# Kernel optimization log

Hardware: AMD Instinct MI355X
Metric: run time of the kernel (lower is better)

## Reference

```python
import jax, jax.numpy as jnp
import numpy as np

N = 100000   # nodes
E = 640000   # edges
G = 256      # graphs in batch
L = 3        # mpnn layers
D_IN = 64    # in_node_channels
E_IN = 16    # in_edge_channels
H = 128      # hidden width (uniform)


def setup_inputs() -> dict:
    key = jax.random.key(0)
    ks = jax.random.split(key, 20)
    s = 0.05
    inp = {
        "x": jax.random.normal(ks[0], (N, D_IN), dtype=jnp.float32),
        "edge_index": jax.random.randint(ks[1], (2, E), 0, N, dtype=jnp.int64),
        "edge_attr": jax.random.normal(ks[2], (E, E_IN), dtype=jnp.float32),
        "batch_vec": jnp.sort(jax.random.randint(ks[3], (N,), 0, G, dtype=jnp.int64)),
        # input encoders
        "Wn0": jax.random.normal(ks[4], (D_IN, H), dtype=jnp.float32) * s,
        "bn0": jnp.zeros((H,), jnp.float32),
        "We0": jax.random.normal(ks[5], (E_IN, H), dtype=jnp.float32) * s,
        "be0": jnp.zeros((H,), jnp.float32),
        # per-layer MPNN params (stacked over L)
        "WM": jax.random.normal(ks[6], (L, 3 * H, H), dtype=jnp.float32) * s,
        "bM": jnp.zeros((L, H), jnp.float32),
        "WU": jax.random.normal(ks[7], (L, 2 * H, H), dtype=jnp.float32) * s,
        "bU": jnp.zeros((L, H), jnp.float32),
        # per-layer node/edge linear layers
        "Wn": jax.random.normal(ks[8], (L, H, H), dtype=jnp.float32) * s,
        "bn": jnp.zeros((L, H), jnp.float32),
        "We": jax.random.normal(ks[9], (L, H, H), dtype=jnp.float32) * s,
        "be": jnp.zeros((L, H), jnp.float32),
        "Wh": jax.random.normal(ks[10], (H, 1), dtype=jnp.float32) * s,
        "bh": jnp.zeros((1,), jnp.float32),
    }
    return inp


def _mpnn_layer(x, edge_attr, src, dst, WM, bM, WU, bU):
    # message: relu(Linear([x_i, x_j, e]))  (x_i = target, x_j = source)
    xi = x[dst]                                   # [E, H]
    xj = x[src]                                   # [E, H]
    m = jax.nn.relu(jnp.concatenate([xi, xj, edge_attr], axis=-1) @ WM + bM)
    # mean aggregation at target nodes
    agg = jax.ops.segment_sum(m, dst, num_segments=N)        # [N, H]
    cnt = jax.ops.segment_sum(jnp.ones((m.shape[0], 1), x.dtype), dst,
                              num_segments=N)
    agg = agg / jnp.maximum(cnt, 1.0)
    # update: relu(Linear([x, aggr_out]))
    return jax.nn.relu(jnp.concatenate([x, agg], axis=-1) @ WU + bU)


def reference(x, edge_index, edge_attr, batch_vec,
              Wn0, bn0, We0, be0, WM, bM, WU, bU, Wn, bn, We, be, Wh, bh):
    src, dst = edge_index[0], edge_index[1]       # PyG source_to_target flow
    h = jax.nn.relu(x @ Wn0 + bn0)                # NodeFeatureLinear
    e = jax.nn.relu(edge_attr @ We0 + be0)        # EdgeFeatureLinear
    for i in range(L):
        h = _mpnn_layer(h, e, src, dst, WM[i], bM[i], WU[i], bU[i])
        h = jax.nn.relu(h @ Wn[i] + bn[i])
        e = jax.nn.relu(e @ We[i] + be[i])
    # global mean pool over graphs
    sums = jax.ops.segment_sum(h, batch_vec, num_segments=G)  # [G, H]
    cnts = jax.ops.segment_sum(jnp.ones((N, 1), h.dtype), batch_vec,
                               num_segments=G)
    pooled = sums / jnp.maximum(cnts, 1.0)
    return pooled @ Wh + bh                       # [G, 1]
```

## Files before the change

### kernel.cpp

```cpp
#include <hip/hip_runtime.h>

#define NN 100000
#define EE 640000
#define GG 256
#define LL 3
#define HH 128

constexpr int BM = 64;
constexpr int BK = 16;

typedef _Float16 f16;
typedef f16 f16x8 __attribute__((ext_vector_type(8)));
typedef f16 f16x4 __attribute__((ext_vector_type(4)));
typedef f16 f16x2 __attribute__((ext_vector_type(2)));
typedef float f32x4 __attribute__((ext_vector_type(4)));

#define TSTR 136

__device__ __forceinline__ void gload_lds16(const void* g, void* l) {
  __builtin_amdgcn_global_load_lds(
      (const __attribute__((address_space(1))) void*)g,
      (__attribute__((address_space(3))) void*)l, 16, 0, 0);
}

template <int MODE>
__global__ __launch_bounds__(256) void gemm_k(
    const float* __restrict__ X, const float* __restrict__ W,
    const float* __restrict__ bias, float* __restrict__ out, int M, int K,
    const float* __restrict__ X2, const float* __restrict__ inv) {
  __shared__ __align__(16) float Xs[BK][BM];
  __shared__ __align__(16) float Ws[BK][HH];

  const int tid = threadIdx.x;
  const int m0 = blockIdx.x * BM;
  const int tm = (tid >> 4) << 2;
  const int tn = (tid & 15) << 3;
  const int xr = tid >> 2;
  const int xc = (tid & 3) << 2;

  float acc[4][8];
#pragma unroll
  for (int i = 0; i < 4; ++i)
#pragma unroll
    for (int j = 0; j < 8; ++j) acc[i][j] = 0.f;

  for (int k0 = 0; k0 < K; k0 += BK) {
    float4 xv = make_float4(0.f, 0.f, 0.f, 0.f);
    if (m0 + xr < M) {
      if (MODE == 3) {
        if (k0 < HH) {
          xv = *(const float4*)(X + (size_t)(m0 + xr) * HH + k0 + xc);
        } else {
          xv = *(const float4*)(X2 + (size_t)(m0 + xr) * HH + (k0 - HH) + xc);
          const float s = inv[m0 + xr];
          xv.x *= s; xv.y *= s; xv.z *= s; xv.w *= s;
        }
      } else {
        xv = *(const float4*)(X + (size_t)(m0 + xr) * K + k0 + xc);
      }
    }
    Xs[xc + 0][xr] = xv.x;
    Xs[xc + 1][xr] = xv.y;
    Xs[xc + 2][xr] = xv.z;
    Xs[xc + 3][xr] = xv.w;
#pragma unroll
    for (int i = 0; i < 2; ++i) {
      const int q = tid + i * 256;
      const int row = q >> 5;
      const int c4 = (q & 31) << 2;
      *(float4*)&Ws[row][c4] =
          *(const float4*)(W + (size_t)(k0 + row) * HH + c4);
    }
    __syncthreads();
#pragma unroll
    for (int k = 0; k < BK; ++k) {
      const float4 x4 = *(const float4*)&Xs[k][tm];
      const float4 w0 = *(const float4*)&Ws[k][tn];
      const float4 w1 = *(const float4*)&Ws[k][tn + 4];
      const float xr_[4] = {x4.x, x4.y, x4.z, x4.w};
      const float wr_[8] = {w0.x, w0.y, w0.z, w0.w, w1.x, w1.y, w1.z, w1.w};
#pragma unroll
      for (int i = 0; i < 4; ++i)
#pragma unroll
        for (int j = 0; j < 8; ++j)
          acc[i][j] = fmaf(xr_[i], wr_[j], acc[i][j]);
    }
    __syncthreads();
  }

#pragma unroll
  for (int i = 0; i < 4; ++i) {
    const int r = m0 + tm + i;
    if (r >= M) continue;
    float o[8];
#pragma unroll
    for (int j = 0; j < 8; ++j) {
      float v = acc[i][j];
      if (MODE == 1 || MODE == 3) {
        v += bias[tn + j];
        v = v > 0.f ? v : 0.f;
      }
      o[j] = v;
    }
    float4* d4 = (float4*)(out + (size_t)r * HH + tn);
    d4[0] = make_float4(o[0], o[1], o[2], o[3]);
    d4[1] = make_float4(o[4], o[5], o[6], o[7]);
  }
}

__global__ void prep_w(const float* __restrict__ We0,
                       const float* __restrict__ We,
                       const float* __restrict__ WM,
                       const float* __restrict__ Wn0,
                       const float* __restrict__ Wn,
                       const float* __restrict__ WU, f16* __restrict__ out) {
  const int buf = blockIdx.x >> 3;
  const int rowg = blockIdx.x & 7;
  const float* src;
  int K;
  if (buf == 0) {
    src = We0; K = 16;
  } else if (buf <= 2) {
    src = We + (size_t)(buf - 1) * HH * HH; K = HH;
  } else if (buf <= 5) {
    src = WM + (size_t)(buf - 3) * 3 * HH * HH + 2 * HH * HH; K = HH;
  } else if (buf == 6) {
    src = Wn0; K = 64;
  } else if (buf <= 9) {
    src = WM + (size_t)(buf - 7) * 3 * HH * HH; K = HH;
  } else if (buf <= 12) {
    src = WM + (size_t)(buf - 10) * 3 * HH * HH + HH * HH; K = HH;
  } else if (buf <= 15) {
    src = Wn + (size_t)(buf - 13) * HH * HH; K = HH;
  } else {
    const int t = buf - 16;
    src = WU + (size_t)(t >> 1) * 2 * HH * HH + (size_t)(t & 1) * HH * HH;
    K = HH;
  }
  f16* dst = out + (size_t)buf * HH * TSTR;
  for (int idx = threadIdx.x; idx < 16 * TSTR; idx += 256) {
    const int n = rowg * 16 + idx / TSTR;
    const int k = idx % TSTR;
    const float v = (k < K) ? src[(size_t)k * HH + n] : 0.f;
    dst[(size_t)n * TSTR + k] = (f16)v;
  }
}

template <int MODE>
__global__ __launch_bounds__(256) void gemm_mfma(
    const float* __restrict__ X, const f16* __restrict__ WT,
    const float* __restrict__ bias, float* __restrict__ out, int M,
    const float* __restrict__ X2, const float* __restrict__ inv,
    const f16* __restrict__ WT2, float* __restrict__ out2) {
  __shared__ __align__(16) char smem[17408 + 34816];
  f16* Xs = (f16*)smem;
  f16* Wt = (f16*)(smem + 17408);
  float* V = (float*)(smem + 17408);

  const int tid = threadIdx.x;
  const int lane = tid & 63;
  const int wv = tid >> 6;
  const int l15 = lane & 15;
  const int q = lane >> 4;
  const int m0 = blockIdx.x * 64;

  f32x4 acc[4][2];
#pragma unroll
  for (int mi = 0; mi < 4; ++mi)
#pragma unroll
    for (int ni = 0; ni < 2; ++ni) {
      f32x4 z = {};
      acc[mi][ni] = z;
    }

  auto stageX = [&](const float* Xp, int stride, int KC, bool scale) {
    const int npr = KC >> 2;
    for (int i = tid; i < 64 * npr; i += 256) {
      const int row = i / npr;
      const int c4 = (i - row * npr) << 2;
      float4 v = make_float4(0.f, 0.f, 0.f, 0.f);
      if (m0 + row < M) {
        v = *(const float4*)(Xp + (size_t)(m0 + row) * stride + c4);
        if (scale) {
          const float s = inv[m0 + row];
          v.x *= s; v.y *= s; v.z *= s; v.w *= s;
        }
      }
      f16x4 hv;
      hv[0] = (f16)v.x; hv[1] = (f16)v.y; hv[2] = (f16)v.z; hv[3] = (f16)v.w;
      *(f16x4*)&Xs[(size_t)row * TSTR + c4] = hv;
    }
  };

  auto stageX16 = [&](const f16* Xp) {
    for (int i = tid; i < 1024; i += 256) {
      const int row = i >> 4;
      const int c8 = (i & 15) << 3;
      f16x8 v = {};
      if (m0 + row < M) v = *(const f16x8*)(Xp + (size_t)(m0 + row) * HH + c8);
      *(f16x8*)&Xs[(size_t)row * TSTR + c8] = v;
    }
  };

  auto stageW = [&](const f16* Wg) {
    const char* g = (const char*)Wg;
    char* l = (char*)Wt;
#pragma unroll
    for (int i = 0; i < 8; ++i)
      gload_lds16(g + tid * 16 + i * 4096, l + tid * 16 + i * 4096);
    if (tid < 128) gload_lds16(g + tid * 16 + 32768, l + tid * 16 + 32768);
  };

  auto mfmaN = [&](f32x4 (&ac)[4][2], int nk) {
    for (int kk = 0; kk < nk; ++kk) {
      f16x8 a[4], b[2];
#pragma unroll
      for (int mi = 0; mi < 4; ++mi)
        a[mi] = *(const f16x8*)&Xs[(size_t)(mi * 16 + l15) * TSTR + kk * 32 +
                                   q * 8];
#pragma unroll
      for (int ni = 0; ni < 2; ++ni)
        b[ni] = *(const f16x8*)&Wt[(size_t)((wv * 2 + ni) * 16 + l15) * TSTR +
                                   kk * 32 + q * 8];
#pragma unroll
      for (int mi = 0; mi < 4; ++mi)
#pragma unroll
        for (int ni = 0; ni < 2; ++ni)
          ac[mi][ni] = __builtin_amdgcn_mfma_f32_16x16x32_f16(
              a[mi], b[ni], ac[mi][ni], 0, 0, 0);
    }
  };

  auto dumpV = [&](f32x4 (&ac)[4][2], const float* bp) {
    float bv0 = 0.f, bv1 = 0.f;
    if (bp) { bv0 = bp[wv * 32 + l15]; bv1 = bp[wv * 32 + 16 + l15]; }
#pragma unroll
    for (int mi = 0; mi < 4; ++mi)
#pragma unroll
      for (int ni = 0; ni < 2; ++ni)
#pragma unroll
        for (int rr = 0; rr < 4; ++rr) {
          float v = ac[mi][ni][rr];
          if (bp) {
            v += ni ? bv1 : bv0;
            v = v > 0.f ? v : 0.f;
          }
          V[(size_t)(mi * 16 + q * 4 + rr) * 132 + wv * 32 + ni * 16 + l15] =
              v;
        }
  };

  auto storeV16 = [&](f16* op) {
    const int tm = (tid >> 4) << 2;
    const int tn = (tid & 15) << 3;
#pragma unroll
    for (int i = 0; i < 4; ++i) {
      const int r = m0 + tm + i;
      if (r >= M) continue;
      const float* vp = &V[(size_t)(tm + i) * 132 + tn];
      f16x8 hv;
#pragma unroll
      for (int j = 0; j < 8; ++j) hv[j] = (f16)vp[j];
      *(f16x8*)(op + (size_t)r * HH + tn) = hv;
    }
  };

  if constexpr (MODE == 2) {
    stageW(WT);
    stageX(X, 64, 64, false);
    __syncthreads();
    mfmaN(acc, 2);
    __syncthreads();
    dumpV(acc, bias);
    __syncthreads();
    storeV16((f16*)out);
  } else if constexpr (MODE == 1) {
    stageW(WT);
    stageX16((const f16*)X);
    __syncthreads();
    mfmaN(acc, 4);
    __syncthreads();
    dumpV(acc, bias);
    __syncthreads();
    storeV16((f16*)out);
  } else if constexpr (MODE == 3) {
    stageW(WT);
    stageX16((const f16*)X);
    __syncthreads();
    mfmaN(acc, 4);
    __syncthreads();
    stageW(WT + (size_t)HH * TSTR);
    stageX(X2, HH, 128, true);
    __syncthreads();
    mfmaN(acc, 4);
    __syncthreads();
    dumpV(acc, bias);
    __syncthreads();
    storeV16((f16*)out);
  } else {
    f32x4 acc2[4][2];
#pragma unroll
    for (int mi = 0; mi < 4; ++mi)
#pragma unroll
      for (int ni = 0; ni < 2; ++ni) {
        f32x4 z = {};
        acc2[mi][ni] = z;
      }
    stageW(WT);
    stageX16((const f16*)X);
    __syncthreads();
    mfmaN(acc, 4);
    __syncthreads();
    stageW(WT2);
    __syncthreads();
    mfmaN(acc2, 4);
    __syncthreads();
    dumpV(acc, nullptr);
    __syncthreads();
    storeV16((f16*)out);
    __syncthreads();
    dumpV(acc2, nullptr);
    __syncthreads();
    storeV16((f16*)out2);
  }
}

template <int CHAIN>
__global__ __launch_bounds__(512) void msg_k(
    const float* __restrict__ ea, const f16* __restrict__ W0T,
    const float* __restrict__ be0, const f16* __restrict__ WeT,
    const float* __restrict__ beL, const f16* __restrict__ WMeT,
    const float* __restrict__ bMl, const f16* __restrict__ A,
    const f16* __restrict__ B, const int* __restrict__ sIdx,
    const int* __restrict__ sSrc, const int* __restrict__ sDst,
    float* __restrict__ agg) {
  __shared__ __align__(16) char smem[34816 + 34816 + 512];
  f16* Tc = (f16*)smem;
  f16* Wc = (f16*)(smem + 34816);
  float* V = (float*)smem;
  int* dstS = (int*)(smem + 69632);

  const int tid = threadIdx.x;
  const int lane = tid & 63;
  const int wv = tid >> 6;
  const int ew = (wv >> 2) * 64;
  const int wn = wv & 3;
  const int l15 = lane & 15;
  const int q = lane >> 4;
  const int r0 = blockIdx.x * 128;

  auto wptr = [&](int p) -> const f16* {
    if (p == 0) return W0T;
    if (p <= CHAIN) return WeT + (size_t)(p - 1) * HH * TSTR;
    return WMeT;
  };

  auto stage_w = [&](const f16* Wg) {
    const char* g = (const char*)Wg;
    char* l = (char*)Wc;
#pragma unroll
    for (int i = 0; i < 4; ++i)
      gload_lds16(g + tid * 16 + i * 8192, l + tid * 16 + i * 8192);
    if (tid < 128) gload_lds16(g + tid * 16 + 32768, l + tid * 16 + 32768);
  };

  stage_w(wptr(0));
  {
    const int xr = tid >> 2;
    const int xc = (tid & 3) << 2;
    const int e = sIdx[r0 + xr];
    const float4 v = *(const float4*)(ea + (size_t)e * 16 + xc);
    f16x4 hv;
    hv[0] = (f16)v.x; hv[1] = (f16)v.y; hv[2] = (f16)v.z; hv[3] = (f16)v.w;
    *(f16x4*)&Tc[(size_t)xr * TSTR + xc] = hv;
    f16x4 z = {};
    *(f16x4*)&Tc[(size_t)xr * TSTR + 16 + xc] = z;
    if (tid < 128) dstS[tid] = sDst[r0 + tid];
  }

  f32x4 acc[4][2];

  auto zero_acc = [&]() {
#pragma unroll
    for (int mi = 0; mi < 4; ++mi)
#pragma unroll
      for (int ni = 0; ni < 2; ++ni) {
        f32x4 z = {};
        acc[mi][ni] = z;
      }
  };

  auto mfma_steps = [&](int nk) {
    for (int kk = 0; kk < nk; ++kk) {
      f16x8 a[4], b[2];
#pragma unroll
      for (int mi = 0; mi < 4; ++mi)
        a[mi] = *(const f16x8*)&Tc[(size_t)(ew + mi * 16 + l15) * TSTR +
                                   kk * 32 + q * 8];
#pragma unroll
      for (int ni = 0; ni < 2; ++ni)
        b[ni] = *(const f16x8*)&Wc[(size_t)((wn * 2 + ni) * 16 + l15) * TSTR +
                                   kk * 32 + q * 8];
#pragma unroll
      for (int mi = 0; mi < 4; ++mi)
#pragma unroll
        for (int ni = 0; ni < 2; ++ni)
          acc[mi][ni] = __builtin_amdgcn_mfma_f32_16x16x32_f16(
              a[mi], b[ni], acc[mi][ni], 0, 0, 0);
    }
  };

  auto relu_body = [&](const float* bias) {
    float bv0 = bias[wn * 32 + l15];
    float bv1 = bias[wn * 32 + 16 + l15];
#pragma unroll
    for (int mi = 0; mi < 4; ++mi)
#pragma unroll
      for (int ni = 0; ni < 2; ++ni) {
        const float bb = ni ? bv1 : bv0;
#pragma unroll
        for (int rr = 0; rr < 4; ++rr) {
          float v = acc[mi][ni][rr] + bb;
          v = v > 0.f ? v : 0.f;
          Tc[(size_t)(ew + mi * 16 + q * 4 + rr) * TSTR + wn * 32 + ni * 16 +
             l15] = (f16)v;
        }
      }
  };

  zero_acc();
  __syncthreads();
  mfma_steps(1);
  __syncthreads();
  stage_w(wptr(1));
  relu_body(be0);
  __syncthreads();

#pragma unroll
  for (int s = 0; s < CHAIN; ++s) {
    zero_acc();
    mfma_steps(4);
    __syncthreads();
    stage_w(wptr(s + 2));
    relu_body(beL + (size_t)s * HH);
    __syncthreads();
  }

  zero_acc();
  mfma_steps(4);
  __syncthreads();

#pragma unroll
  for (int mi = 0; mi < 4; ++mi)
#pragma unroll
    for (int ni = 0; ni < 2; ++ni)
#pragma unroll
      for (int rr = 0; rr < 4; ++rr)
        V[(size_t)(ew + mi * 16 + q * 4 + rr) * 129 + wn * 32 + ni * 16 +
          l15] = acc[mi][ni][rr];
  __syncthreads();

  const int tm = (tid >> 4) << 2;
  const int tn = (tid & 15) << 3;
  const float4 m0v = *(const float4*)(bMl + tn);
  const float4 m1v = *(const float4*)(bMl + tn + 4);
  const float mv[8] = {m0v.x, m0v.y, m0v.z, m0v.w,
                       m1v.x, m1v.y, m1v.z, m1v.w};
#pragma unroll
  for (int i = 0; i < 4; ++i) {
    const int rr = r0 + tm + i;
    const int d = dstS[tm + i];
    const int s = sSrc[rr];
    const f16x8 a8 = *(const f16x8*)(A + (size_t)d * HH + tn);
    const f16x8 b8 = *(const f16x8*)(B + (size_t)s * HH + tn);
    float* vp = &V[(size_t)(tm + i) * 129 + tn];
#pragma unroll
    for (int j = 0; j < 8; ++j)
      vp[j] = fmaxf(vp[j] + (float)a8[j] + (float)b8[j] + mv[j], 0.f);
  }
  __syncthreads();

  const int c = tid & 127;
  const int h = tid >> 7;
  float racc = 0.f;
  int cur = dstS[h * 32];
  bool first = true;
  for (int e2 = h * 32; e2 < h * 32 + 32; ++e2) {
    const int d = dstS[e2];
    if (d != cur) {
      if (first) {
        atomicAdd(&agg[(size_t)cur * HH + c], racc);
        first = false;
      } else {
        agg[(size_t)cur * HH + c] = racc;
      }
      racc = 0.f;
      cur = d;
    }
    racc += V[(size_t)e2 * 129 + c];
  }
  atomicAdd(&agg[(size_t)cur * HH + c], racc);
}

__global__ void count_kernel(const int* __restrict__ dst, int* cnt, int E) {
  const int i = blockIdx.x * 256 + threadIdx.x;
  if (i < E) atomicAdd(&cnt[dst[i]], 1);
}

__global__ void invcnt_kernel(const int* __restrict__ cnt, float* inv, int n) {
  const int i = blockIdx.x * 256 + threadIdx.x;
  if (i < n) inv[i] = 1.0f / (float)max(cnt[i], 1);
}

__global__ void scan_block(const int* __restrict__ cnt, int* excl, int* bsum,
                           int n) {
  __shared__ int s[256];
  const int tx = threadIdx.x;
  const int i = blockIdx.x * 256 + tx;
  const int v = (i < n) ? cnt[i] : 0;
  s[tx] = v;
  __syncthreads();
  for (int off = 1; off < 256; off <<= 1) {
    int tv = (tx >= off) ? s[tx - off] : 0;
    __syncthreads();
    s[tx] += tv;
    __syncthreads();
  }
  if (i < n) excl[i] = s[tx] - v;
  if (tx == 255) bsum[blockIdx.x] = s[255];
}

__global__ __launch_bounds__(512) void scan_bsum(int* bsum, int nb) {
  __shared__ int s[512];
  const int t = threadIdx.x;
  const int v0 = (t < nb) ? bsum[t] : 0;
  s[t] = v0;
  __syncthreads();
  for (int off = 1; off < 512; off <<= 1) {
    const int tv = (t >= off) ? s[t - off] : 0;
    __syncthreads();
    s[t] += tv;
    __syncthreads();
  }
  if (t < nb) bsum[t] = s[t] - v0;
}

__global__ void scan_add(int* excl, const int* __restrict__ bsum, int n) {
  const int i = blockIdx.x * 256 + threadIdx.x;
  if (i < n) excl[i] += bsum[blockIdx.x];
}

__global__ void scatter_edges(const int* __restrict__ dst,
                              const int* __restrict__ src,
                              const int* __restrict__ off, int* ctr, int* sIdx,
                              int* sSrc, int* sDst, int E) {
  const int e = blockIdx.x * 256 + threadIdx.x;
  if (e >= E) return;
  const int d = dst[e];
  const int p = off[d] + atomicAdd(&ctr[d], 1);
  sIdx[p] = e;
  sSrc[p] = src[e];
  sDst[p] = d;
}

__global__ void pool_accum(const f16* __restrict__ h,
                           const int* __restrict__ batch,
                           float* __restrict__ gsum, int M) {
  const int col = threadIdx.x;
  const int r0 = blockIdx.x * 64;
  const int rend = min(r0 + 64, M);
  if (r0 >= M) return;
  float acc = 0.f;
  int cur = batch[r0];
  for (int r = r0; r < rend; ++r) {
    const int b = batch[r];
    if (b != cur) {
      atomicAdd(&gsum[(size_t)cur * HH + col], acc);
      acc = 0.f;
      cur = b;
    }
    acc += (float)h[(size_t)r * HH + col];
  }
  atomicAdd(&gsum[(size_t)cur * HH + col], acc);
}

__global__ void gcnt_kernel(const int* __restrict__ batch, int* gcnt, int n) {
  const int i = blockIdx.x * 256 + threadIdx.x;
  if (i < n) atomicAdd(&gcnt[batch[i]], 1);
}

__global__ void head_kernel(const float* __restrict__ gsum,
                            const int* __restrict__ gcnt,
                            const float* __restrict__ Wh,
                            const float* __restrict__ bh,
                            float* __restrict__ out) {
  const int g = blockIdx.x;
  const int t = threadIdx.x;
  float v = gsum[(size_t)g * HH + t] * Wh[t];
#pragma unroll
  for (int o = 32; o > 0; o >>= 1) v += __shfl_down(v, o, 64);
  __shared__ float red[2];
  if ((t & 63) == 0) red[t >> 6] = v;
  __syncthreads();
  if (t == 0) {
    const float s = red[0] + red[1];
    const float c = (float)max(gcnt[g], 1);
    out[g] = s / c + bh[0];
  }
}

extern "C" void kernel_launch(void* const* d_in, const int* in_sizes, int n_in,
                              void* d_out, int out_size, void* d_ws,
                              size_t ws_size, hipStream_t stream) {
  (void)in_sizes; (void)n_in; (void)out_size;
  const float* x = (const float*)d_in[0];
  const int* ei = (const int*)d_in[1];
  const float* ea = (const float*)d_in[2];
  const int* batch = (const int*)d_in[3];
  const float* Wn0 = (const float*)d_in[4];
  const float* bn0 = (const float*)d_in[5];
  const float* We0 = (const float*)d_in[6];
  const float* be0 = (const float*)d_in[7];
  const float* WM = (const float*)d_in[8];
  const float* bM = (const float*)d_in[9];
  const float* WU = (const float*)d_in[10];
  const float* bU = (const float*)d_in[11];
  const float* Wn = (const float*)d_in[12];
  const float* bn = (const float*)d_in[13];
  const float* We = (const float*)d_in[14];
  const float* be = (const float*)d_in[15];
  const float* Wh = (const float*)d_in[16];
  const float* bh = (const float*)d_in[17];

  const int* srcI = ei;
  const int* dstI = ei + EE;

  float* w = (float*)d_ws;
  size_t o = 0;
  f16* h16 = (f16*)(w + o);  o += (size_t)NN * HH / 2;
  float* agg = w + o;  o += (size_t)NN * HH;
  f16* A16 = (f16*)(w + o); o += (size_t)NN * HH / 2;
  f16* B16 = (f16*)(w + o); o += (size_t)NN * HH / 2;
  float* gsum = w + o; o += (size_t)GG * HH;
  float* invc = w + o; o += (size_t)NN;
  int* cnt = (int*)(w + o);  o += (size_t)NN;
  int* gcnt = (int*)(w + o); o += (size_t)GG;
  int* off = (int*)(w + o);  o += (size_t)NN;
  int* ctr = (int*)(w + o);  o += (size_t)NN;
  int* bsum = (int*)(w + o); o += 512;
  int* sIdx = (int*)(w + o); o += (size_t)EE;
  int* sSrc = (int*)(w + o); o += (size_t)EE;
  int* sDst = (int*)(w + o); o += (size_t)EE;
  f16* Wp = (f16*)(w + o);   o += (size_t)22 * HH * TSTR / 2;
  if (o * sizeof(float) > ws_size) return;

  auto WB = [&](int i) { return Wp + (size_t)i * HH * TSTR; };

  const dim3 blk(256);
  const int gridN = (NN + BM - 1) / BM;
  const int gridE = EE / 128;
  const int NBLK = (NN + 255) / 256;

  hipMemsetAsync(cnt, 0, (size_t)NN * sizeof(int), stream);
  hipMemsetAsync(ctr, 0, (size_t)NN * sizeof(int), stream);
  hipMemsetAsync(gsum, 0, (size_t)GG * HH * sizeof(float), stream);
  hipMemsetAsync(gcnt, 0, (size_t)GG * sizeof(int), stream);

  count_kernel<<<(EE + 255) / 256, blk, 0, stream>>>(dstI, cnt, EE);
  scan_block<<<NBLK, blk, 0, stream>>>(cnt, off, bsum, NN);
  scan_bsum<<<1, dim3(512), 0, stream>>>(bsum, NBLK);
  scan_add<<<NBLK, blk, 0, stream>>>(off, bsum, NN);
  scatter_edges<<<(EE + 255) / 256, blk, 0, stream>>>(dstI, srcI, off, ctr,
                                                      sIdx, sSrc, sDst, EE);
  invcnt_kernel<<<(NN + 255) / 256, blk, 0, stream>>>(cnt, invc, NN);
  prep_w<<<22 * 8, blk, 0, stream>>>(We0, We, WM, Wn0, Wn, WU, Wp);

  gemm_mfma<2><<<gridN, blk, 0, stream>>>(x, WB(6), bn0, (float*)h16, NN,
                                          nullptr, nullptr, nullptr, nullptr);

  for (int l = 0; l < LL; ++l) {
    gemm_mfma<4><<<gridN, blk, 0, stream>>>((const float*)h16, WB(7 + l),
                                            nullptr, (float*)A16, NN, nullptr,
                                            nullptr, WB(10 + l), (float*)B16);
    hipMemsetAsync(agg, 0, (size_t)NN * HH * sizeof(float), stream);
    switch (l) {
      case 0:
        msg_k<0><<<gridE, dim3(512), 0, stream>>>(
            ea, WB(0), be0, WB(1), be, WB(3), bM + 0 * HH, A16, B16, sIdx,
            sSrc, sDst, agg);
        break;
      case 1:
        msg_k<1><<<gridE, dim3(512), 0, stream>>>(
            ea, WB(0), be0, WB(1), be, WB(4), bM + 1 * HH, A16, B16, sIdx,
            sSrc, sDst, agg);
        break;
      default:
        msg_k<2><<<gridE, dim3(512), 0, stream>>>(
            ea, WB(0), be0, WB(1), be, WB(5), bM + 2 * HH, A16, B16, sIdx,
            sSrc, sDst, agg);
        break;
    }
    gemm_mfma<3><<<gridN, blk, 0, stream>>>((const float*)h16,
                                            WB(16 + 2 * l), bU + l * HH,
                                            (float*)h16, NN, agg, invc,
                                            nullptr, nullptr);
    gemm_mfma<1><<<gridN, blk, 0, stream>>>((const float*)h16, WB(13 + l),
                                            bn + l * HH, (float*)h16, NN,
                                            nullptr, nullptr, nullptr,
                                            nullptr);
  }

  pool_accum<<<gridN, dim3(128), 0, stream>>>(h16, batch, gsum, NN);
  gcnt_kernel<<<(NN + 255) / 256, blk, 0, stream>>>(batch, gcnt, NN);
  head_kernel<<<GG, dim3(128), 0, stream>>>(gsum, gcnt, Wh, bh, (float*)d_out);
}
```

Baseline: 1.035 ms.

## Fuse node GEMM chain (update, node linear, next-layer projections) into one kernel

Replaces the separate per-layer node GEMM launches (update, node linear, next layer's A/B projections) with one fused kernel per layer, plus a fused encoder+projection kernel. Intermediate h stays in LDS as fp16 between GEMMs instead of round-tripping through global memory, and kernel launches drop. Each block now runs more sequential GEMM stages with extra barriers, and the in-place h16 write-back relies on row-local dependence only.

```diff
diff --git a/kernel.cpp b/kernel.cpp
--- a/kernel.cpp
+++ b/kernel.cpp
@@ -21,91 +21,6 @@
   __builtin_amdgcn_global_load_lds(
       (const __attribute__((address_space(1))) void*)g,
       (__attribute__((address_space(3))) void*)l, 16, 0, 0);
-}
-
-template <int MODE>
-__global__ __launch_bounds__(256) void gemm_k(
-    const float* __restrict__ X, const float* __restrict__ W,
-    const float* __restrict__ bias, float* __restrict__ out, int M, int K,
-    const float* __restrict__ X2, const float* __restrict__ inv) {
-  __shared__ __align__(16) float Xs[BK][BM];
-  __shared__ __align__(16) float Ws[BK][HH];
-
-  const int tid = threadIdx.x;
-  const int m0 = blockIdx.x * BM;
-  const int tm = (tid >> 4) << 2;
-  const int tn = (tid & 15) << 3;
-  const int xr = tid >> 2;
-  const int xc = (tid & 3) << 2;
-
-  float acc[4][8];
-#pragma unroll
-  for (int i = 0; i < 4; ++i)
-#pragma unroll
-    for (int j = 0; j < 8; ++j) acc[i][j] = 0.f;
-
-  for (int k0 = 0; k0 < K; k0 += BK) {
-    float4 xv = make_float4(0.f, 0.f, 0.f, 0.f);
-    if (m0 + xr < M) {
-      if (MODE == 3) {
-        if (k0 < HH) {
-          xv = *(const float4*)(X + (size_t)(m0 + xr) * HH + k0 + xc);
-        } else {
-          xv = *(const float4*)(X2 + (size_t)(m0 + xr) * HH + (k0 - HH) + xc);
-          const float s = inv[m0 + xr];
-          xv.x *= s; xv.y *= s; xv.z *= s; xv.w *= s;
-        }
-      } else {
-        xv = *(const float4*)(X + (size_t)(m0 + xr) * K + k0 + xc);
-      }
-    }
-    Xs[xc + 0][xr] = xv.x;
-    Xs[xc + 1][xr] = xv.y;
-    Xs[xc + 2][xr] = xv.z;
-    Xs[xc + 3][xr] = xv.w;
-#pragma unroll
-    for (int i = 0; i < 2; ++i) {
-      const int q = tid + i * 256;
-      const int row = q >> 5;
-      const int c4 = (q & 31) << 2;
-      *(float4*)&Ws[row][c4] =
-          *(const float4*)(W + (size_t)(k0 + row) * HH + c4);
-    }
-    __syncthreads();
-#pragma unroll
-    for (int k = 0; k < BK; ++k) {
-      const float4 x4 = *(const float4*)&Xs[k][tm];
-      const float4 w0 = *(const float4*)&Ws[k][tn];
-      const float4 w1 = *(const float4*)&Ws[k][tn + 4];
-      const float xr_[4] = {x4.x, x4.y, x4.z, x4.w};
-      const float wr_[8] = {w0.x, w0.y, w0.z, w0.w, w1.x, w1.y, w1.z, w1.w};
-#pragma unroll
-      for (int i = 0; i < 4; ++i)
-#pragma unroll
-        for (int j = 0; j < 8; ++j)
-          acc[i][j] = fmaf(xr_[i], wr_[j], acc[i][j]);
-    }
-    __syncthreads();
-  }
-
-#pragma unroll
-  for (int i = 0; i < 4; ++i) {
-    const int r = m0 + tm + i;
-    if (r >= M) continue;
-    float o[8];
-#pragma unroll
-    for (int j = 0; j < 8; ++j) {
-      float v = acc[i][j];
-      if (MODE == 1 || MODE == 3) {
-        v += bias[tn + j];
-        v = v > 0.f ? v : 0.f;
-      }
-      o[j] = v;
-    }
-    float4* d4 = (float4*)(out + (size_t)r * HH + tn);
-    d4[0] = make_float4(o[0], o[1], o[2], o[3]);
-    d4[1] = make_float4(o[4], o[5], o[6], o[7]);
-  }
 }
 
 __global__ void prep_w(const float* __restrict__ We0,
@@ -146,183 +61,227 @@
   }
 }
 
-template <int MODE>
-__global__ __launch_bounds__(256) void gemm_mfma(
-    const float* __restrict__ X, const f16* __restrict__ WT,
-    const float* __restrict__ bias, float* __restrict__ out, int M,
-    const float* __restrict__ X2, const float* __restrict__ inv,
-    const f16* __restrict__ WT2, float* __restrict__ out2) {
-  __shared__ __align__(16) char smem[17408 + 34816];
-  f16* Xs = (f16*)smem;
-  f16* Wt = (f16*)(smem + 17408);
-  float* V = (float*)(smem + 17408);
-
-  const int tid = threadIdx.x;
-  const int lane = tid & 63;
-  const int wv = tid >> 6;
-  const int l15 = lane & 15;
-  const int q = lane >> 4;
-  const int m0 = blockIdx.x * 64;
-
-  f32x4 acc[4][2];
+struct GemmCtx {
+  f16* Xs; f16* Wt; float* V;
+  int tid, lane, wv, l15, q, m0;
+};
+
+__device__ __forceinline__ void ctx_init(GemmCtx& c, char* smem) {
+  c.Xs = (f16*)smem;
+  c.Wt = (f16*)(smem + 17408);
+  c.V = (float*)(smem + 17408);
+  c.tid = threadIdx.x;
+  c.lane = c.tid & 63;
+  c.wv = c.tid >> 6;
+  c.l15 = c.lane & 15;
+  c.q = c.lane >> 4;
+  c.m0 = blockIdx.x * 64;
+}
+
+__device__ __forceinline__ void c_stageW(GemmCtx& c, const f16* Wg) {
+  const char* g = (const char*)Wg;
+  char* l = (char*)c.Wt;
+#pragma unroll
+  for (int i = 0; i < 8; ++i)
+    gload_lds16(g + c.tid * 16 + i * 4096, l + c.tid * 16 + i * 4096);
+  if (c.tid < 128) gload_lds16(g + c.tid * 16 + 32768, l + c.tid * 16 + 32768);
+}
+
+__device__ __forceinline__ void c_stageXf32(GemmCtx& c, const float* Xp,
+                                            int stride, int KC, bool scale,
+                                            const float* inv, int M) {
+  const int npr = KC >> 2;
+  for (int i = c.tid; i < 64 * npr; i += 256) {
+    const int row = i / npr;
+    const int c4 = (i - row * npr) << 2;
+    float4 v = make_float4(0.f, 0.f, 0.f, 0.f);
+    if (c.m0 + row < M) {
+      v = *(const float4*)(Xp + (size_t)(c.m0 + row) * stride + c4);
+      if (scale) {
+        const float s = inv[c.m0 + row];
+        v.x *= s; v.y *= s; v.z *= s; v.w *= s;
+      }
+    }
+    f16x4 hv;
+    hv[0] = (f16)v.x; hv[1] = (f16)v.y; hv[2] = (f16)v.z; hv[3] = (f16)v.w;
+    *(f16x4*)&c.Xs[(size_t)row * TSTR + c4] = hv;
+  }
+}
+
+__device__ __forceinline__ void c_stageX16(GemmCtx& c, const f16* Xp, int M) {
+  for (int i = c.tid; i < 1024; i += 256) {
+    const int row = i >> 4;
+    const int c8 = (i & 15) << 3;
+    f16x8 v = {};
+    if (c.m0 + row < M) v = *(const f16x8*)(Xp + (size_t)(c.m0 + row) * HH + c8);
+    *(f16x8*)&c.Xs[(size_t)row * TSTR + c8] = v;
+  }
+}
+
+__device__ __forceinline__ void c_mfmaN(GemmCtx& c, f32x4 (&ac)[4][2],
+                                        int nk) {
+  for (int kk = 0; kk < nk; ++kk) {
+    f16x8 a[4], b[2];
+#pragma unroll
+    for (int mi = 0; mi < 4; ++mi)
+      a[mi] = *(const f16x8*)&c.Xs[(size_t)(mi * 16 + c.l15) * TSTR + kk * 32 +
+                                   c.q * 8];
+#pragma unroll
+    for (int ni = 0; ni < 2; ++ni)
+      b[ni] = *(const f16x8*)&c.Wt[(size_t)((c.wv * 2 + ni) * 16 + c.l15) *
+                                       TSTR +
+                                   kk * 32 + c.q * 8];
+#pragma unroll
+    for (int mi = 0; mi < 4; ++mi)
+#pragma unroll
+      for (int ni = 0; ni < 2; ++ni)
+        ac[mi][ni] = __builtin_amdgcn_mfma_f32_16x16x32_f16(a[mi], b[ni],
+                                                            ac[mi][ni], 0, 0,
+                                                            0);
+  }
+}
+
+__device__ __forceinline__ void c_zero(f32x4 (&ac)[4][2]) {
 #pragma unroll
   for (int mi = 0; mi < 4; ++mi)
 #pragma unroll
     for (int ni = 0; ni < 2; ++ni) {
       f32x4 z = {};
-      acc[mi][ni] = z;
-    }
-
-  auto stageX = [&](const float* Xp, int stride, int KC, bool scale) {
-    const int npr = KC >> 2;
-    for (int i = tid; i < 64 * npr; i += 256) {
-      const int row = i / npr;
-      const int c4 = (i - row * npr) << 2;
-      float4 v = make_float4(0.f, 0.f, 0.f, 0.f);
-      if (m0 + row < M) {
-        v = *(const float4*)(Xp + (size_t)(m0 + row) * stride + c4);
-        if (scale) {
-          const float s = inv[m0 + row];
-          v.x *= s; v.y *= s; v.z *= s; v.w *= s;
-        }
+      ac[mi][ni] = z;
+    }
+}
+
+__device__ __forceinline__ void c_reluXs(GemmCtx& c, f32x4 (&ac)[4][2],
+                                         const float* bias) {
+  const float bv0 = bias[c.wv * 32 + c.l15];
+  const float bv1 = bias[c.wv * 32 + 16 + c.l15];
+#pragma unroll
+  for (int mi = 0; mi < 4; ++mi)
+#pragma unroll
+    for (int ni = 0; ni < 2; ++ni) {
+      const float bb = ni ? bv1 : bv0;
+#pragma unroll
+      for (int rr = 0; rr < 4; ++rr) {
+        float v = ac[mi][ni][rr] + bb;
+        v = v > 0.f ? v : 0.f;
+        c.Xs[(size_t)(mi * 16 + c.q * 4 + rr) * TSTR + c.wv * 32 + ni * 16 +
+             c.l15] = (f16)v;
       }
-      f16x4 hv;
-      hv[0] = (f16)v.x; hv[1] = (f16)v.y; hv[2] = (f16)v.z; hv[3] = (f16)v.w;
-      *(f16x4*)&Xs[(size_t)row * TSTR + c4] = hv;
-    }
-  };
-
-  auto stageX16 = [&](const f16* Xp) {
-    for (int i = tid; i < 1024; i += 256) {
-      const int row = i >> 4;
-      const int c8 = (i & 15) << 3;
-      f16x8 v = {};
-      if (m0 + row < M) v = *(const f16x8*)(Xp + (size_t)(m0 + row) * HH + c8);
-      *(f16x8*)&Xs[(size_t)row * TSTR + c8] = v;
-    }
-  };
-
-  auto stageW = [&](const f16* Wg) {
-    const char* g = (const char*)Wg;
-    char* l = (char*)Wt;
-#pragma unroll
-    for (int i = 0; i < 8; ++i)
-      gload_lds16(g + tid * 16 + i * 4096, l + tid * 16 + i * 4096);
-    if (tid < 128) gload_lds16(g + tid * 16 + 32768, l + tid * 16 + 32768);
-  };
-
-  auto mfmaN = [&](f32x4 (&ac)[4][2], int nk) {
-    for (int kk = 0; kk < nk; ++kk) {
-      f16x8 a[4], b[2];
-#pragma unroll
-      for (int mi = 0; mi < 4; ++mi)
-        a[mi] = *(const f16x8*)&Xs[(size_t)(mi * 16 + l15) * TSTR + kk * 32 +
-                                   q * 8];
-#pragma unroll
-      for (int ni = 0; ni < 2; ++ni)
-        b[ni] = *(const f16x8*)&Wt[(size_t)((wv * 2 + ni) * 16 + l15) * TSTR +
-                                   kk * 32 + q * 8];
-#pragma unroll
-      for (int mi = 0; mi < 4; ++mi)
-#pragma unroll
-        for (int ni = 0; ni < 2; ++ni)
-          ac[mi][ni] = __builtin_amdgcn_mfma_f32_16x16x32_f16(
-              a[mi], b[ni], ac[mi][ni], 0, 0, 0);
-    }
-  };
-
-  auto dumpV = [&](f32x4 (&ac)[4][2], const float* bp) {
-    float bv0 = 0.f, bv1 = 0.f;
-    if (bp) { bv0 = bp[wv * 32 + l15]; bv1 = bp[wv * 32 + 16 + l15]; }
-#pragma unroll
-    for (int mi = 0; mi < 4; ++mi)
-#pragma unroll
-      for (int ni = 0; ni < 2; ++ni)
-#pragma unroll
-        for (int rr = 0; rr < 4; ++rr) {
-          float v = ac[mi][ni][rr];
-          if (bp) {
-            v += ni ? bv1 : bv0;
-            v = v > 0.f ? v : 0.f;
-          }
-          V[(size_t)(mi * 16 + q * 4 + rr) * 132 + wv * 32 + ni * 16 + l15] =
-              v;
-        }
-  };
-
-  auto storeV16 = [&](f16* op) {
-    const int tm = (tid >> 4) << 2;
-    const int tn = (tid & 15) << 3;
-#pragma unroll
-    for (int i = 0; i < 4; ++i) {
-      const int r = m0 + tm + i;
-      if (r >= M) continue;
-      const float* vp = &V[(size_t)(tm + i) * 132 + tn];
-      f16x8 hv;
-#pragma unroll
-      for (int j = 0; j < 8; ++j) hv[j] = (f16)vp[j];
-      *(f16x8*)(op + (size_t)r * HH + tn) = hv;
-    }
-  };
-
-  if constexpr (MODE == 2) {
-    stageW(WT);
-    stageX(X, 64, 64, false);
-    __syncthreads();
-    mfmaN(acc, 2);
-    __syncthreads();
-    dumpV(acc, bias);
-    __syncthreads();
-    storeV16((f16*)out);
-  } else if constexpr (MODE == 1) {
-    stageW(WT);
-    stageX16((const f16*)X);
-    __syncthreads();
-    mfmaN(acc, 4);
-    __syncthreads();
-    dumpV(acc, bias);
-    __syncthreads();
-    storeV16((f16*)out);
-  } else if constexpr (MODE == 3) {
-    stageW(WT);
-    stageX16((const f16*)X);
-    __syncthreads();
-    mfmaN(acc, 4);
-    __syncthreads();
-    stageW(WT + (size_t)HH * TSTR);
-    stageX(X2, HH, 128, true);
-    __syncthreads();
-    mfmaN(acc, 4);
-    __syncthreads();
-    dumpV(acc, bias);
-    __syncthreads();
-    storeV16((f16*)out);
-  } else {
-    f32x4 acc2[4][2];
-#pragma unroll
-    for (int mi = 0; mi < 4; ++mi)
-#pragma unroll
-      for (int ni = 0; ni < 2; ++ni) {
-        f32x4 z = {};
-        acc2[mi][ni] = z;
-      }
-    stageW(WT);
-    stageX16((const f16*)X);
-    __syncthreads();
-    mfmaN(acc, 4);
-    __syncthreads();
-    stageW(WT2);
-    __syncthreads();
-    mfmaN(acc2, 4);
-    __syncthreads();
-    dumpV(acc, nullptr);
-    __syncthreads();
-    storeV16((f16*)out);
-    __syncthreads();
-    dumpV(acc2, nullptr);
-    __syncthreads();
-    storeV16((f16*)out2);
-  }
+    }
+}
+
+__device__ __forceinline__ void c_dumpV(GemmCtx& c, f32x4 (&ac)[4][2]) {
+#pragma unroll
+  for (int mi = 0; mi < 4; ++mi)
+#pragma unroll
+    for (int ni = 0; ni < 2; ++ni)
+#pragma unroll
+      for (int rr = 0; rr < 4; ++rr)
+        c.V[(size_t)(mi * 16 + c.q * 4 + rr) * 132 + c.wv * 32 + ni * 16 +
+            c.l15] = ac[mi][ni][rr];
+}
+
+__device__ __forceinline__ void c_storeV16(GemmCtx& c, f16* op, int M) {
+  const int tm = (c.tid >> 4) << 2;
+  const int tn = (c.tid & 15) << 3;
+#pragma unroll
+  for (int i = 0; i < 4; ++i) {
+    const int r = c.m0 + tm + i;
+    if (r >= M) continue;
+    const float* vp = &c.V[(size_t)(tm + i) * 132 + tn];
+    f16x8 hv;
+#pragma unroll
+    for (int j = 0; j < 8; ++j) hv[j] = (f16)vp[j];
+    *(f16x8*)(op + (size_t)r * HH + tn) = hv;
+  }
+}
+
+__device__ __forceinline__ void c_storeXs16(GemmCtx& c, f16* op, int M) {
+  const int tm = (c.tid >> 4) << 2;
+  const int tn = (c.tid & 15) << 3;
+#pragma unroll
+  for (int i = 0; i < 4; ++i) {
+    const int r = c.m0 + tm + i;
+    if (r >= M) continue;
+    *(f16x8*)(op + (size_t)r * HH + tn) =
+        *(const f16x8*)&c.Xs[(size_t)(tm + i) * TSTR + tn];
+  }
+}
+
+__device__ __forceinline__ void c_projAB(GemmCtx& c, f32x4 (&ac)[4][2],
+                                         const f16* WA, const f16* WBp,
+                                         f16* A16, f16* B16, int M) {
+  c_zero(ac);
+  c_mfmaN(c, ac, 4);
+  __syncthreads();
+  c_dumpV(c, ac);
+  __syncthreads();
+  c_storeV16(c, A16, M);
+  __syncthreads();
+  c_stageW(c, WBp);
+  __syncthreads();
+  c_zero(ac);
+  c_mfmaN(c, ac, 4);
+  __syncthreads();
+  c_dumpV(c, ac);
+  __syncthreads();
+  c_storeV16(c, B16, M);
+}
+
+__global__ __launch_bounds__(256) void fused_enc(
+    const float* __restrict__ x, const f16* __restrict__ Wn0T,
+    const float* __restrict__ bn0, f16* __restrict__ h16,
+    const f16* __restrict__ WA, const f16* __restrict__ WBp,
+    f16* __restrict__ A16, f16* __restrict__ B16, int M) {
+  __shared__ __align__(16) char smem[17408 + 34816];
+  GemmCtx c; ctx_init(c, smem);
+  f32x4 acc[4][2];
+  c_zero(acc);
+  c_stageW(c, Wn0T);
+  c_stageXf32(c, x, 64, 64, false, nullptr, M);
+  __syncthreads();
+  c_mfmaN(c, acc, 2);
+  __syncthreads();
+  c_reluXs(c, acc, bn0);
+  c_stageW(c, WA);
+  __syncthreads();
+  c_storeXs16(c, h16, M);
+  c_projAB(c, acc, WA, WBp, A16, B16, M);
+}
+
+template <int HAS_AB>
+__global__ __launch_bounds__(256) void fused_upd(
+    const f16* __restrict__ h, const f16* __restrict__ WU01,
+    const float* __restrict__ bU, const float* __restrict__ agg,
+    const float* __restrict__ invc, const f16* __restrict__ WnT,
+    const float* __restrict__ bn, const f16* __restrict__ WA,
+    const f16* __restrict__ WBp, f16* __restrict__ hout,
+    f16* __restrict__ A16, f16* __restrict__ B16, int M) {
+  __shared__ __align__(16) char smem[17408 + 34816];
+  GemmCtx c; ctx_init(c, smem);
+  f32x4 acc[4][2];
+  c_zero(acc);
+  c_stageW(c, WU01);
+  c_stageX16(c, h, M);
+  __syncthreads();
+  c_mfmaN(c, acc, 4);
+  __syncthreads();
+  c_stageW(c, WU01 + (size_t)HH * TSTR);
+  c_stageXf32(c, agg, HH, 128, true, invc, M);
+  __syncthreads();
+  c_mfmaN(c, acc, 4);
+  __syncthreads();
+  c_reluXs(c, acc, bU);
+  c_stageW(c, WnT);
+  __syncthreads();
+  c_zero(acc);
+  c_mfmaN(c, acc, 4);
+  __syncthreads();
+  c_reluXs(c, acc, bn);
+  if (HAS_AB) c_stageW(c, WA);
+  __syncthreads();
+  c_storeXs16(c, hout, M);
+  if (HAS_AB) c_projAB(c, acc, WA, WBp, A16, B16, M);
 }
 
 template <int CHAIN>
@@ -675,13 +634,10 @@
   invcnt_kernel<<<(NN + 255) / 256, blk, 0, stream>>>(cnt, invc, NN);
   prep_w<<<22 * 8, blk, 0, stream>>>(We0, We, WM, Wn0, Wn, WU, Wp);
 
-  gemm_mfma<2><<<gridN, blk, 0, stream>>>(x, WB(6), bn0, (float*)h16, NN,
-                                          nullptr, nullptr, nullptr, nullptr);
+  fused_enc<<<gridN, blk, 0, stream>>>(x, WB(6), bn0, h16, WB(7), WB(10),
+                                       A16, B16, NN);
 
   for (int l = 0; l < LL; ++l) {
-    gemm_mfma<4><<<gridN, blk, 0, stream>>>((const float*)h16, WB(7 + l),
-                                            nullptr, (float*)A16, NN, nullptr,
-                                            nullptr, WB(10 + l), (float*)B16);
     hipMemsetAsync(agg, 0, (size_t)NN * HH * sizeof(float), stream);
     switch (l) {
       case 0:
@@ -700,14 +656,15 @@
             sSrc, sDst, agg);
         break;
     }
-    gemm_mfma<3><<<gridN, blk, 0, stream>>>((const float*)h16,
-                                            WB(16 + 2 * l), bU + l * HH,
-                                            (float*)h16, NN, agg, invc,
-                                            nullptr, nullptr);
-    gemm_mfma<1><<<gridN, blk, 0, stream>>>((const float*)h16, WB(13 + l),
-                                            bn + l * HH, (float*)h16, NN,
-                                            nullptr, nullptr, nullptr,
-                                            nullptr);
+    if (l < LL - 1) {
+      fused_upd<1><<<gridN, blk, 0, stream>>>(
+          h16, WB(16 + 2 * l), bU + l * HH, agg, invc, WB(13 + l), bn + l * HH,
+          WB(7 + l + 1), WB(10 + l + 1), h16, A16, B16, NN);
+    } else {
+      fused_upd<0><<<gridN, blk, 0, stream>>>(
+          h16, WB(16 + 2 * l), bU + l * HH, agg, invc, WB(13 + l), bn + l * HH,
+          nullptr, nullptr, h16, nullptr, nullptr, NN);
+    }
   }
 
   pool_accum<<<gridN, dim3(128), 0, stream>>>(h16, batch, gsum, NN);
```

New measurement: 985.2 us. 4.8% less time.
